# Kernel tuning notes

Hardware: AMD Instinct MI355X
Metric: run time of the kernel (lower is better)

Reference implementation:

```python
import jax, jax.numpy as jnp
import numpy as np

NB, HD, NL, NF = 5, 64, 4, 10           # num_bins, hidden_dim(d_model), num_layers, num_frames
DI, DS, DC, DTR = 128, 16, 4, 4          # d_inner=2*HD, d_state, d_conv, dt_rank=ceil(HD/16)
B, H, W = 4, 64, 64


def _conv2d(x, w, b):
    y = jax.lax.conv_general_dilated(x, w, (1, 1), 'SAME',
                                     dimension_numbers=('NCHW', 'OIHW', 'NCHW'))
    return y + b[None, :, None, None]


def _bn_relu(x, gamma, beta, eps=1e-5):
    # BatchNorm2d in training mode: biased batch stats over (N,H,W)
    mean = x.mean(axis=(0, 2, 3), keepdims=True)
    var = x.var(axis=(0, 2, 3), keepdims=True)
    y = (x - mean) * jax.lax.rsqrt(var + eps)
    return jax.nn.relu(y * gamma[None, :, None, None] + beta[None, :, None, None])


def _silu(x):
    return x * jax.nn.sigmoid(x)


def _causal_dwconv(x, w, b):
    # x: (B,L,DI), w: (DI,K) depthwise causal conv, b: (DI,)
    K = w.shape[1]
    L = x.shape[1]
    xp = jnp.pad(x, ((0, 0), (K - 1, 0), (0, 0)))
    y = sum(xp[:, k:k + L, :] * w[:, k] for k in range(K))
    return y + b


def _selective_scan(u, delta, A, Bm, Cm, D):
    # u,delta: (B,L,DI); A: (DI,DS); Bm,Cm: (B,L,DS); D: (DI,)
    dT, BT, CT, uT = (t.transpose(1, 0, 2) for t in (delta, Bm, Cm, u))
    h0 = jnp.zeros((u.shape[0], A.shape[0], A.shape[1]), u.dtype)

    def step(h, inp):
        d_t, B_t, C_t, u_t = inp                     # (B,DI),(B,DS),(B,DS),(B,DI)
        dA = jnp.exp(d_t[:, :, None] * A)            # (B,DI,DS)
        h = dA * h + (d_t * u_t)[:, :, None] * B_t[:, None, :]
        y = jnp.einsum('bds,bs->bd', h, C_t)
        return h, y

    _, ys = jax.lax.scan(step, h0, (dT, BT, CT, uT))  # ys: (L,B,DI)
    return ys.transpose(1, 0, 2) + u * D


def _mamba(x, in_proj, conv_w, conv_b, x_proj, dt_w, dt_b, A_log, Dp, out_proj):
    xz = x @ in_proj.T                               # (B,L,2*DI)
    xi, z = jnp.split(xz, 2, axis=-1)
    xi = _silu(_causal_dwconv(xi, conv_w, conv_b))
    xdbc = xi @ x_proj.T                             # (B,L,DTR+2*DS)
    dt, Bm, Cm = jnp.split(xdbc, [DTR, DTR + DS], axis=-1)
    delta = jax.nn.softplus(dt @ dt_w.T + dt_b)
    A = -jnp.exp(A_log)
    y = _selective_scan(xi, delta, A, Bm, Cm, Dp)
    return (y * _silu(z)) @ out_proj.T


def setup_inputs() -> dict:
    key = jax.random.key(0)
    ks = jax.random.split(key, 20)
    s = 0.02
    inp = {
        'x': jax.random.normal(ks[0], (B, NB, H, W), jnp.float32),
        'enc_w': jax.random.normal(ks[1], (HD, NB, 3, 3), jnp.float32) * s,
        'enc_b': jnp.zeros((HD,), jnp.float32),
        'enc_g': jnp.ones((HD,), jnp.float32),
        'enc_be': jnp.zeros((HD,), jnp.float32),
        'in_proj': jax.random.normal(ks[2], (NL, 2 * DI, HD), jnp.float32) * s,
        'conv_w': jax.random.normal(ks[3], (NL, DI, DC), jnp.float32) * s,
        'conv_b': jnp.zeros((NL, DI), jnp.float32),
        'x_proj': jax.random.normal(ks[4], (NL, DTR + 2 * DS, DI), jnp.float32) * s,
        'dt_w': jax.random.normal(ks[5], (NL, DI, DTR), jnp.float32) * s,
        'dt_b': jax.random.normal(ks[6], (NL, DI), jnp.float32) * 0.1 - 4.0,
        'A_log': jnp.broadcast_to(jnp.log(jnp.arange(1, DS + 1, dtype=jnp.float32)),
                                  (NL, DI, DS)).copy(),
        'Dp': jnp.ones((NL, DI), jnp.float32),
        'out_proj': jax.random.normal(ks[7], (NL, HD, DI), jnp.float32) * s,
        'dec1_w': jax.random.normal(ks[8], (HD, HD, 3, 3), jnp.float32) * s,
        'dec1_b': jnp.zeros((HD,), jnp.float32),
        'dec1_g': jnp.ones((HD,), jnp.float32),
        'dec1_be': jnp.zeros((HD,), jnp.float32),
        'dec2_w': jax.random.normal(ks[9], (NF, HD, 3, 3), jnp.float32) * s,
        'dec2_b': jnp.zeros((NF,), jnp.float32),
    }
    return inp


def reference(x, enc_w, enc_b, enc_g, enc_be, in_proj, conv_w, conv_b, x_proj,
              dt_w, dt_b, A_log, Dp, out_proj, dec1_w, dec1_b, dec1_g, dec1_be,
              dec2_w, dec2_b):
    Bb, _, Hh, Ww = x.shape
    h = _bn_relu(_conv2d(x, enc_w, enc_b), enc_g, enc_be)   # (B,HD,H,W)
    t = h.reshape(Bb, HD, Hh * Ww).transpose(0, 2, 1)        # (B,L,HD)
    for i in range(NL):
        t = t + _mamba(t, in_proj[i], conv_w[i], conv_b[i], x_proj[i],
                       dt_w[i], dt_b[i], A_log[i], Dp[i], out_proj[i])
    h = t.transpose(0, 2, 1).reshape(Bb, HD, Hh, Ww)
    h = _bn_relu(_conv2d(h, dec1_w, dec1_b), dec1_g, dec1_be)
    return _conv2d(h, dec2_w, dec2_b)                        # (B,NF,H,W)
```

## Files before the change

kernel.cpp:

```cpp
#include <hip/hip_runtime.h>
#include <hip/hip_bf16.h>

#define BB   4
#define NBC  5
#define HD   64
#define NLAYER 4
#define NFC  10
#define DIM  128
#define DSN  16
#define DCN  4
#define DTRK 4
#define HH   64
#define WWD  64
#define LL   4096
#define MM   (BB*LL)
#define SUB    16
#define NSUB   256
#define WIN    19

__global__ void k_prep_all(const float* __restrict__ in_proj, const float* __restrict__ out_proj,
                           const float* __restrict__ dec1_w, const float* __restrict__ dec2_w,
                           float* __restrict__ wTin, float* __restrict__ wTout,
                           float* __restrict__ wT1, float* __restrict__ wT2,
                           float* __restrict__ stats, float* __restrict__ stats2) {
    int idx = blockIdx.x * blockDim.x + threadIdx.x;
    if (idx < 65536) {
        int n = idx & 255, k = (idx >> 8) & 63, l = idx >> 14;
        wTin[idx] = in_proj[(l << 14) + (n << 6) + k];
    } else if (idx < 98304) {
        int j = idx - 65536;
        int n = j & 63, k = (j >> 6) & 127, l = j >> 13;
        wTout[j] = out_proj[(l << 13) + (n << 7) + k];
    } else if (idx < 135168) {
        int j = idx - 98304;
        int co = j & 63, tap = (j >> 6) % 9, ci = j / 576;
        wT1[j] = dec1_w[co * 576 + ci * 9 + tap];
    } else if (idx < 142848) {
        int j = idx - 135168;
        int tap = j % 12, t2 = j / 12, co = t2 % NFC, ci = t2 / NFC;
        wT2[j] = (tap < 9) ? dec2_w[co * 576 + ci * 9 + tap] : 0.f;
    } else if (idx < 143104) {
        int j = idx - 142848;
        if (j < 128) stats[j] = 0.f; else stats2[j - 128] = 0.f;
    }
}

__global__ void k_enc_conv(const float* __restrict__ x, const float* __restrict__ w,
                           const float* __restrict__ bias, float* __restrict__ out,
                           float* __restrict__ stats) {
    __shared__ float r1[256], r2[256];
    int tid = threadIdx.x;
// ... 64 lines not shown
    int rg = tid >> 5;
    int cg = tid & 31;
    float acc[8][8] = {};
    int n0 = cg << 3;
    for (int k4 = 0; k4 < 16; ++k4) {
        float4 a[8];
        #pragma unroll
        for (int r2 = 0; r2 < 8; ++r2)
            a[r2] = *(const float4*)&ts[((rg << 3) + r2) * 68 + (k4 << 2)];
        #pragma unroll
        for (int kk = 0; kk < 4; ++kk) {
            const float* wr = wT + (((k4 << 2) + kk) << 8) + n0;
            float4 w0 = *(const float4*)&wr[0];
            float4 w1 = *(const float4*)&wr[4];
            #pragma unroll
            for (int r2 = 0; r2 < 8; ++r2) {
                float av = (kk == 0) ? a[r2].x : (kk == 1) ? a[r2].y
                         : (kk == 2) ? a[r2].z : a[r2].w;
                acc[r2][0] += av * w0.x; acc[r2][1] += av * w0.y;
                acc[r2][2] += av * w0.z; acc[r2][3] += av * w0.w;
                acc[r2][4] += av * w1.x; acc[r2][5] += av * w1.y;
                acc[r2][6] += av * w1.z; acc[r2][7] += av * w1.w;
            }
        }
    }
    #pragma unroll
    for (int r2 = 0; r2 < 8; ++r2) {
        long m = m0 + (rg << 3) + r2;
        *(float4*)&xz[(m << 8) + n0]     = make_float4(acc[r2][0], acc[r2][1], acc[r2][2], acc[r2][3]);
        *(float4*)&xz[(m << 8) + n0 + 4] = make_float4(acc[r2][4], acc[r2][5], acc[r2][6], acc[r2][7]);
    }
}

__global__ __launch_bounds__(256, 3) void k_xproj_fused(
        const float* __restrict__ xz, const float* __restrict__ cw,
        const float* __restrict__ cb, const float* __restrict__ Wx,
        const float* __restrict__ dw, const float* __restrict__ dbias,
        const float* __restrict__ A_log,
        float* __restrict__ xi, float* __restrict__ delta,
        float* __restrict__ xdbc, float* __restrict__ Pb, float* __restrict__ Sb) {
    __shared__ __align__(16) float xz_s[WIN * 128];
    __shared__ __align__(16) float xi_s[SUB * 128];
    __shared__ __align__(16) float w_s[36 * 132];
    __shared__ __align__(16) float xs[SUB * 36];
    long m0 = (long)blockIdx.x << 4;
    int l0 = (int)(m0 & 4095);
    int b = (int)(m0 >> 12);
    int sc = l0 >> 4;
    int tid = threadIdx.x;

    for (int i = tid; i < WIN * 32; i += 256) {
        int j = i >> 5, c4 = (i & 31) << 2;
        float4 v = make_float4(0.f, 0.f, 0.f, 0.f);
        int l = l0 - 3 + j;
        if (l >= 0) v = *(const float4*)&xz[(m0 - 3 + j) * 256 + c4];
        *(float4*)&xz_s[j * 128 + c4] = v;
    }
    for (int i = tid; i < 1152; i += 256) {
        int n = i >> 5, c4 = (i & 31) << 2;
        *(float4*)&w_s[n * 132 + c4] = *(const float4*)&Wx[(n << 7) + c4];
    }
    int d4c = (tid & 31) << 2;
    float4 cwv0 = *(const float4*)&cw[(d4c + 0) << 2];
    float4 cwv1 = *(const float4*)&cw[(d4c + 1) << 2];
    float4 cwv2 = *(const float4*)&cw[(d4c + 2) << 2];
    float4 cwv3 = *(const float4*)&cw[(d4c + 3) << 2];
    float4 cbv  = *(const float4*)&cb[d4c];
    __syncthreads();

    #pragma unroll
    for (int ii = 0; ii < 2; ++ii) {
        int r = (tid >> 5) + (ii << 3);
        float4 x0 = *(const float4*)&xz_s[(r + 0) * 128 + d4c];
        float4 x1 = *(const float4*)&xz_s[(r + 1) * 128 + d4c];
        float4 x2 = *(const float4*)&xz_s[(r + 2) * 128 + d4c];
        float4 x3 = *(const float4*)&xz_s[(r + 3) * 128 + d4c];
        float4 a;
        a.x = cbv.x + x0.x * cwv0.x + x1.x * cwv0.y + x2.x * cwv0.z + x3.x * cwv0.w;
        a.y = cbv.y + x0.y * cwv1.x + x1.y * cwv1.y + x2.y * cwv1.z + x3.y * cwv1.w;
        a.z = cbv.z + x0.z * cwv2.x + x1.z * cwv2.y + x2.z * cwv2.z + x3.z * cwv2.w;
        a.w = cbv.w + x0.w * cwv3.x + x1.w * cwv3.y + x2.w * cwv3.z + x3.w * cwv3.w;
        a.x = a.x / (1.f + __expf(-a.x));
        a.y = a.y / (1.f + __expf(-a.y));
        a.z = a.z / (1.f + __expf(-a.z));
        a.w = a.w / (1.f + __expf(-a.w));
        *(float4*)&xi_s[r * 128 + d4c] = a;
        *(float4*)&xi[(m0 + r) * 128 + d4c] = a;
    }
    __syncthreads();

    {
        int n = tid & 63, rg6 = tid >> 6;
        if (n < 36) {
            float acc[4] = {0, 0, 0, 0};
            for (int k4 = 0; k4 < 32; ++k4) {
                float4 w4 = *(const float4*)&w_s[n * 132 + (k4 << 2)];
                #pragma unroll
                for (int r = 0; r < 4; ++r) {
                    float4 a4 = *(const float4*)&xi_s[((rg6 << 2) + r) * 128 + (k4 << 2)];
                    acc[r] += a4.x * w4.x + a4.y * w4.y + a4.z * w4.z + a4.w * w4.w;
                }
            }
            #pragma unroll
            for (int r = 0; r < 4; ++r) {
                int rr = (rg6 << 2) + r;
                xdbc[(m0 + rr) * 36 + n] = acc[r];
                xs[rr * 36 + n] = acc[r];
            }
        }
    }
    __syncthreads();

    float* delta_s = xz_s;
    for (int i = tid; i < SUB * 128; i += 256) {
        int r = i >> 7, di2 = i & 127;
        float4 d4 = *(const float4*)&dw[di2 << 2];
        float v = dbias[di2]
                + xs[r * 36 + 0] * d4.x + xs[r * 36 + 1] * d4.y
                + xs[r * 36 + 2] * d4.z + xs[r * 36 + 3] * d4.w;
        float sp = (v > 20.f) ? v : log1pf(expf(v));
        delta_s[r * 128 + di2] = sp;
        delta[(m0 + r) * 128 + di2] = sp;
    }
    __syncthreads();

    {
        int di = tid >> 1;
        int dso = (tid & 1) << 3;
        float4 al0 = *(const float4*)&A_log[(di << 4) + dso];
        float4 al1 = *(const float4*)&A_log[(di << 4) + dso + 4];
        float Av[8] = { -expf(al0.x), -expf(al0.y), -expf(al0.z), -expf(al0.w),
                        -expf(al1.x), -expf(al1.y), -expf(al1.z), -expf(al1.w) };
        float h[8] = {0,0,0,0,0,0,0,0};
        float P[8] = {1,1,1,1,1,1,1,1};
        #pragma unroll 4
        for (int i = 0; i < SUB; ++i) {
            float d = delta_s[i * 128 + di];
            float u = xi_s[i * 128 + di];
            float du = d * u;
            float4 B0 = *(const float4*)&xs[i * 36 + DTRK + dso];
            float4 B1 = *(const float4*)&xs[i * 36 + DTRK + dso + 4];
            float a0 = __expf(d * Av[0]); h[0] = a0 * h[0] + du * B0.x; P[0] *= a0;
            float a1 = __expf(d * Av[1]); h[1] = a1 * h[1] + du * B0.y; P[1] *= a1;
            float a2 = __expf(d * Av[2]); h[2] = a2 * h[2] + du * B0.z; P[2] *= a2;
            float a3 = __expf(d * Av[3]); h[3] = a3 * h[3] + du * B0.w; P[3] *= a3;
            float a4 = __expf(d * Av[4]); h[4] = a4 * h[4] + du * B1.x; P[4] *= a4;
            float a5 = __expf(d * Av[5]); h[5] = a5 * h[5] + du * B1.y; P[5] *= a5;
            float a6 = __expf(d * Av[6]); h[6] = a6 * h[6] + du * B1.z; P[6] *= a6;
            float a7 = __expf(d * Av[7]); h[7] = a7 * h[7] + du * B1.w; P[7] *= a7;
        }
        long o = (((long)(b * NSUB + sc)) << 11) + (di << 4) + dso;
        *(float4*)&Pb[o]     = make_float4(P[0], P[1], P[2], P[3]);
        *(float4*)&Pb[o + 4] = make_float4(P[4], P[5], P[6], P[7]);
        *(float4*)&Sb[o]     = make_float4(h[0], h[1], h[2], h[3]);
        *(float4*)&Sb[o + 4] = make_float4(h[4], h[5], h[6], h[7]);
    }
}

__global__ void k_scan_p2(const float* __restrict__ Pb, float* Sb) {
    int t = blockIdx.x * blockDim.x + threadIdx.x;
    int b = t >> 11;
    int s = t & 2047;
    long base = ((long)b * NSUB) << 11;
    float p[4], sv[4];
    #pragma unroll
    for (int k = 0; k < 4; ++k) {
        long idx = base + ((long)k << 11) + s;
        p[k] = Pb[idx]; sv[k] = Sb[idx];
    }
    float h = 0.f;
    for (int c = 0; c < 64; ++c) {
        float np[4] = {0, 0, 0, 0}, ns[4] = {0, 0, 0, 0};
        if (c < 63) {
            #pragma unroll
            for (int k = 0; k < 4; ++k) {
                long idx = base + ((long)(((c + 1) << 2) + k) << 11) + s;
                np[k] = Pb[idx]; ns[k] = Sb[idx];
            }
        }
        long i0 = base + ((long)(c << 2) << 11) + s;
        Sb[i0]        = h;  h = p[0] * h + sv[0];
        Sb[i0 + 2048] = h;  h = p[1] * h + sv[1];
        Sb[i0 + 4096] = h;  h = p[2] * h + sv[2];
        Sb[i0 + 6144] = h;  h = p[3] * h + sv[3];
        #pragma unroll
        for (int k = 0; k < 4; ++k) { p[k] = np[k]; sv[k] = ns[k]; }
    }
}

__global__ __launch_bounds__(256, 4) void k_scan_p3_oi(
        float* xz, const float* __restrict__ xi, const float* __restrict__ delta,
        const float* __restrict__ xdbc,
        const float* __restrict__ A_log, const float* __restrict__ Dp,
        const float* __restrict__ wTo, const float* __restrict__ wTi,
        float* __restrict__ tio, const float* __restrict__ h0g, int doB) {
    __shared__ __align__(16) float d_s[SUB * 128];
    __shared__ __align__(16) float u_s[SUB * 132];
    __shared__ __align__(16) float bc_s[SUB * 36];
    __shared__ __align__(16) float t_s[SUB * 68];
    long m0 = (long)blockIdx.x << 4;
    int tid = threadIdx.x;
    int fb = blockIdx.x;

    for (int i = tid; i < SUB * 32; i += 256) {
        int r = i >> 5, c4 = (i & 31) << 2;
        *(float4*)&d_s[r * 128 + c4] = *(const float4*)&delta[(m0 + r) * 128 + c4];
        *(float4*)&u_s[r * 132 + c4] = *(const float4*)&xi[(m0 + r) * 128 + c4];
    }
    for (int i = tid; i < SUB * 9; i += 256) {
        int r = i / 9, c4 = (i - r * 9) << 2;
        *(float4*)&bc_s[r * 36 + c4] = *(const float4*)&xdbc[(m0 + r) * 36 + c4];
    }
    int di = tid >> 1;
    int dso = (tid & 1) << 3;
    float4 al0 = *(const float4*)&A_log[(di << 4) + dso];
    float4 al1 = *(const float4*)&A_log[(di << 4) + dso + 4];
    float Av[8] = { -expf(al0.x), -expf(al0.y), -expf(al0.z), -expf(al0.w),
                    -expf(al1.x), -expf(al1.y), -expf(al1.z), -expf(al1.w) };
    float Dv = Dp[di];
    long o = (((long)fb) << 11) + (di << 4) + dso;
    float4 h04 = *(const float4*)&h0g[o];
    float4 h14 = *(const float4*)&h0g[o + 4];
    float h[8] = { h04.x, h04.y, h04.z, h04.w, h14.x, h14.y, h14.z, h14.w };
    __syncthreads();

    #pragma unroll 4
    for (int i = 0; i < SUB; ++i) {
        float d = d_s[i * 128 + di];
        float u = u_s[i * 132 + di];
        float du = d * u;
        const float* bc = &bc_s[i * 36];
        float4 B0 = *(const float4*)&bc[DTRK + dso];
        float4 B1 = *(const float4*)&bc[DTRK + dso + 4];
        float4 C0 = *(const float4*)&bc[DTRK + DSN + dso];
        float4 C1 = *(const float4*)&bc[DTRK + DSN + dso + 4];
        float a0 = __expf(d * Av[0]); h[0] = a0 * h[0] + du * B0.x;
        float a1 = __expf(d * Av[1]); h[1] = a1 * h[1] + du * B0.y;
        float a2 = __expf(d * Av[2]); h[2] = a2 * h[2] + du * B0.z;
        float a3 = __expf(d * Av[3]); h[3] = a3 * h[3] + du * B0.w;
        float a4 = __expf(d * Av[4]); h[4] = a4 * h[4] + du * B1.x;
        float a5 = __expf(d * Av[5]); h[5] = a5 * h[5] + du * B1.y;
        float a6 = __expf(d * Av[6]); h[6] = a6 * h[6] + du * B1.z;
        float a7 = __expf(d * Av[7]); h[7] = a7 * h[7] + du * B1.w;
        float yp = h[0] * C0.x + h[1] * C0.y + h[2] * C0.z + h[3] * C0.w
                 + h[4] * C1.x + h[5] * C1.y + h[6] * C1.z + h[7] * C1.w;
        yp += __shfl_xor(yp, 1);
        if (dso == 0)
            u_s[i * 132 + di] = yp + u * Dv;
    }
    __syncthreads();

    for (int i = tid; i < SUB * 32; i += 256) {
        int r = i >> 5, c4 = (i & 31) << 2;
        float4 y4 = *(float4*)&u_s[r * 132 + c4];
        float4 z4 = *(const float4*)&xz[((m0 + r) << 8) + DIM + c4];
        y4.x *= z4.x / (1.f + __expf(-z4.x));
        y4.y *= z4.y / (1.f + __expf(-z4.y));
        y4.z *= z4.z / (1.f + __expf(-z4.z));
        y4.w *= z4.w / (1.f + __expf(-z4.w));
        *(float4*)&u_s[r * 132 + c4] = y4;
    }
    __syncthreads();

    {
        int rg = tid >> 4, cg = tid & 15;
        int n0 = cg << 2;
        float acc4[4] = {};
        for (int k4 = 0; k4 < 32; ++k4) {
            float4 a0 = *(const float4*)&u_s[rg * 132 + (k4 << 2)];
            #pragma unroll
            for (int kk = 0; kk < 4; ++kk) {
                const float* wr = wTo + (((k4 << 2) + kk) << 6) + n0;
                float4 w0 = *(const float4*)&wr[0];
                float av = (kk == 0) ? a0.x : (kk == 1) ? a0.y : (kk == 2) ? a0.z : a0.w;
                acc4[0] += av * w0.x; acc4[1] += av * w0.y;
                acc4[2] += av * w0.z; acc4[3] += av * w0.w;
            }
        }
        long m = m0 + rg;
        float4 tv = *(const float4*)&tio[(m << 6) + n0];
        tv.x += acc4[0]; tv.y += acc4[1];
        tv.z += acc4[2]; tv.w += acc4[3];
        *(float4*)&tio[(m << 6) + n0] = tv;
        *(float4*)&t_s[rg * 68 + n0] = tv;
    }
    if (!doB) return;
    __syncthreads();

    {
        int rg = tid >> 5, cgn = tid & 31;
        int n0 = cgn << 3;
        float acc[2][8] = {};
        for (int k4 = 0; k4 < 16; ++k4) {
            float4 a[2];
            a[0] = *(const float4*)&t_s[(rg << 1) * 68 + (k4 << 2)];
            a[1] = *(const float4*)&t_s[((rg << 1) + 1) * 68 + (k4 << 2)];
            #pragma unroll
            for (int kk = 0; kk < 4; ++kk) {
                const float* wr = wTi + (((k4 << 2) + kk) << 8) + n0;
                float4 w0 = *(const float4*)&wr[0];
                float4 w1 = *(const float4*)&wr[4];
                #pragma unroll
                for (int r2 = 0; r2 < 2; ++r2) {
                    float av = (kk == 0) ? a[r2].x : (kk == 1) ? a[r2].y
                             : (kk == 2) ? a[r2].z : a[r2].w;
                    acc[r2][0] += av * w0.x; acc[r2][1] += av * w0.y;
                    acc[r2][2] += av * w0.z; acc[r2][3] += av * w0.w;
                    acc[r2][4] += av * w1.x; acc[r2][5] += av * w1.y;
                    acc[r2][6] += av * w1.z; acc[r2][7] += av * w1.w;
                }
            }
        }
        #pragma unroll
        for (int r2 = 0; r2 < 2; ++r2) {
            long m = m0 + (rg << 1) + r2;
            *(float4*)&xz[(m << 8) + n0]     = make_float4(acc[r2][0], acc[r2][1], acc[r2][2], acc[r2][3]);
            *(float4*)&xz[(m << 8) + n0 + 4] = make_float4(acc[r2][4], acc[r2][5], acc[r2][6], acc[r2][7]);
        }
    }
}

__global__ __launch_bounds__(256, 1) void k_dec1_new(const float* __restrict__ tin,
                                                     const float* __restrict__ wT,
                                                     const float* __restrict__ bias,
                                                     float* __restrict__ out,
                                                     float* __restrict__ stats2) {
    __shared__ __align__(16) float x_s[64 * 132];
    __shared__ __align__(16) float w_s[4 * 4608];
    int tile = blockIdx.x;
    int b = blockIdx.y;
    int ty0 = (tile >> 3) << 3;
    int tx0 = (tile & 7) << 3;
    int tid = threadIdx.x;
    int wv = tid >> 6;
    int lane = tid & 63;
    int r = lane >> 3;
    int cg = lane & 7;

    for (int i = tid; i < 6400; i += 256) {
        int pl = i >> 6;
        int c = i & 63;
        int py = pl / 10, px = pl - py * 10;
        int ih = ty0 + py - 1, iw = tx0 + px - 1;
        float v = 0.f;
        if (ih >= 0 && ih < HH && iw >= 0 && iw < WWD)
            v = tin[(((long)((b << 12) + (ih << 6) + iw)) << 6) + c];
        x_s[c * 132 + py * 12 + px] = v;
    }
    float* myw = &w_s[wv * 4608];
    const float* gw = wT + (wv * 16) * 576;
    float4 pref[18];
// ... 166 lines not shown
    const float* x       = (const float*)d_in[0];
    const float* enc_w   = (const float*)d_in[1];
    const float* enc_b   = (const float*)d_in[2];
    const float* enc_g   = (const float*)d_in[3];
    const float* enc_be  = (const float*)d_in[4];
    const float* in_proj = (const float*)d_in[5];
    const float* conv_w  = (const float*)d_in[6];
    const float* conv_b  = (const float*)d_in[7];
    const float* x_proj  = (const float*)d_in[8];
    const float* dt_w    = (const float*)d_in[9];
    const float* dt_b    = (const float*)d_in[10];
    const float* A_log   = (const float*)d_in[11];
    const float* Dp      = (const float*)d_in[12];
    const float* out_prj = (const float*)d_in[13];
    const float* dec1_w  = (const float*)d_in[14];
    const float* dec1_b  = (const float*)d_in[15];
    const float* dec1_g  = (const float*)d_in[16];
    const float* dec1_be = (const float*)d_in[17];
    const float* dec2_w  = (const float*)d_in[18];
    const float* dec2_b  = (const float*)d_in[19];
    float* out = (float*)d_out;

    float* ws = (float*)d_ws;
    size_t off = 0;
    float* conv_buf  = ws + off; off += 1048576;
    float* stats     = ws + off; off += 128;
    float* stats2    = ws + off; off += 128;
    float* wT1       = ws + off; off += 36864;
    float* wT2       = ws + off; off += 7680;
    float* wTin      = ws + off; off += 65536;
    float* wTout     = ws + off; off += 32768;
    float* t_buf     = ws + off; off += 1048576;
    float* xz_buf    = ws + off; off += 4194304;
    float* xi_buf    = ws + off; off += 2097152;
    float* delta_buf = ws + off; off += 2097152;
    float* xdbc_buf  = ws + off; off += 589824;
    float* Pb        = ws + off; off += 2097152;
    float* Sb        = ws + off; off += 2097152;
    (void)ws_size; (void)in_sizes; (void)n_in; (void)out_size;

    k_prep_all<<<560, 256, 0, stream>>>(in_proj, out_prj, dec1_w, dec2_w,
                                        wTin, wTout, wT1, wT2, stats, stats2);

    k_enc_conv<<<4096, 256, 0, stream>>>(x, enc_w, enc_b, conv_buf, stats);

    k_gemm_in_bn<<<256, 256, 0, stream>>>(conv_buf, stats, enc_g, enc_be, wTin,
                                          t_buf, xz_buf);

    for (int i = 0; i < NLAYER; ++i) {
        int doB = (i < NLAYER - 1) ? 1 : 0;
        k_xproj_fused<<<1024, 256, 0, stream>>>(
            xz_buf, conv_w + i * DIM * DCN, conv_b + i * DIM, x_proj + i * 36 * DIM,
            dt_w + i * DIM * DTRK, dt_b + i * DIM, A_log + i * DIM * DSN,
            xi_buf, delta_buf, xdbc_buf, Pb, Sb);
        k_scan_p2<<<32, 256, 0, stream>>>(Pb, Sb);
        k_scan_p3_oi<<<1024, 256, 0, stream>>>(
            xz_buf, xi_buf, delta_buf, xdbc_buf,
            A_log + i * DIM * DSN, Dp + i * DIM,
            wTout + i * 8192, wTin + ((i + 1) & 3) * 16384,
            t_buf, Sb, doB);
    }

    dim3 dg1(64, BB);
    k_dec1_new<<<dg1, 256, 0, stream>>>(t_buf, wT1, dec1_b, conv_buf, stats2);
    k_dec2_fused<<<dg1, 256, 0, stream>>>(conv_buf, stats2, dec1_g, dec1_be, wT2, dec2_b, out);
}
```

Measured before the change: 547.4 us.

## Halve scan chunk size to double block count and fuse gating into scan loop

Shrinks the per-block sequence chunk from 16 to 8 rows, so the x-projection and scan-output kernels launch twice as many blocks. The x_proj weight staging in shared memory is dropped in favour of direct global reads, and occupancy hints are raised. The SiLU(z) gating is folded into the scan loop using a preloaded z tile, which removes a separate pass and a barrier. In exchange, the serial carry-propagation kernel walks twice as many chunks, the prefix buffers double in size, and weight reuse per block falls.

```diff
diff --git a/kernel.cpp b/kernel.cpp
--- a/kernel.cpp
+++ b/kernel.cpp
@@ -14,9 +14,9 @@
 #define WWD  64
 #define LL   4096
 #define MM   (BB*LL)
-#define SUB    16
-#define NSUB   256
-#define WIN    19
+#define SUB    8
+#define NSUB   512
+#define WIN    11
 
 __global__ void k_prep_all(const float* __restrict__ in_proj, const float* __restrict__ out_proj,
                            const float* __restrict__ dec1_w, const float* __restrict__ dec2_w,
@@ -147,7 +147,7 @@
     }
 }
 
-__global__ __launch_bounds__(256, 3) void k_xproj_fused(
+__global__ __launch_bounds__(256, 4) void k_xproj_fused(
         const float* __restrict__ xz, const float* __restrict__ cw,
         const float* __restrict__ cb, const float* __restrict__ Wx,
         const float* __restrict__ dw, const float* __restrict__ dbias,
@@ -156,12 +156,9 @@
         float* __restrict__ xdbc, float* __restrict__ Pb, float* __restrict__ Sb) {
     __shared__ __align__(16) float xz_s[WIN * 128];
     __shared__ __align__(16) float xi_s[SUB * 128];
-    __shared__ __align__(16) float w_s[36 * 132];
     __shared__ __align__(16) float xs[SUB * 36];
-    long m0 = (long)blockIdx.x << 4;
+    long m0 = (long)blockIdx.x << 3;
     int l0 = (int)(m0 & 4095);
-    int b = (int)(m0 >> 12);
-    int sc = l0 >> 4;
     int tid = threadIdx.x;
 
     for (int i = tid; i < WIN * 32; i += 256) {
@@ -171,10 +168,6 @@
         if (l >= 0) v = *(const float4*)&xz[(m0 - 3 + j) * 256 + c4];
         *(float4*)&xz_s[j * 128 + c4] = v;
     }
-    for (int i = tid; i < 1152; i += 256) {
-        int n = i >> 5, c4 = (i & 31) << 2;
-        *(float4*)&w_s[n * 132 + c4] = *(const float4*)&Wx[(n << 7) + c4];
-    }
     int d4c = (tid & 31) << 2;
     float4 cwv0 = *(const float4*)&cw[(d4c + 0) << 2];
     float4 cwv1 = *(const float4*)&cw[(d4c + 1) << 2];
@@ -183,9 +176,8 @@
     float4 cbv  = *(const float4*)&cb[d4c];
     __syncthreads();
 
-    #pragma unroll
-    for (int ii = 0; ii < 2; ++ii) {
-        int r = (tid >> 5) + (ii << 3);
+    {
+        int r = tid >> 5;
         float4 x0 = *(const float4*)&xz_s[(r + 0) * 128 + d4c];
         float4 x1 = *(const float4*)&xz_s[(r + 1) * 128 + d4c];
         float4 x2 = *(const float4*)&xz_s[(r + 2) * 128 + d4c];
@@ -207,18 +199,18 @@
     {
         int n = tid & 63, rg6 = tid >> 6;
         if (n < 36) {
-            float acc[4] = {0, 0, 0, 0};
+            float acc[2] = {0, 0};
             for (int k4 = 0; k4 < 32; ++k4) {
-                float4 w4 = *(const float4*)&w_s[n * 132 + (k4 << 2)];
+                float4 w4 = *(const float4*)&Wx[(n << 7) + (k4 << 2)];
                 #pragma unroll
-                for (int r = 0; r < 4; ++r) {
-                    float4 a4 = *(const float4*)&xi_s[((rg6 << 2) + r) * 128 + (k4 << 2)];
+                for (int r = 0; r < 2; ++r) {
+                    float4 a4 = *(const float4*)&xi_s[((rg6 << 1) + r) * 128 + (k4 << 2)];
                     acc[r] += a4.x * w4.x + a4.y * w4.y + a4.z * w4.z + a4.w * w4.w;
                 }
             }
             #pragma unroll
-            for (int r = 0; r < 4; ++r) {
-                int rr = (rg6 << 2) + r;
+            for (int r = 0; r < 2; ++r) {
+                int rr = (rg6 << 1) + r;
                 xdbc[(m0 + rr) * 36 + n] = acc[r];
                 xs[rr * 36 + n] = acc[r];
             }
@@ -248,7 +240,7 @@
                         -expf(al1.x), -expf(al1.y), -expf(al1.z), -expf(al1.w) };
         float h[8] = {0,0,0,0,0,0,0,0};
         float P[8] = {1,1,1,1,1,1,1,1};
-        #pragma unroll 4
+        #pragma unroll
         for (int i = 0; i < SUB; ++i) {
             float d = delta_s[i * 128 + di];
             float u = xi_s[i * 128 + di];
@@ -264,7 +256,7 @@
             float a6 = __expf(d * Av[6]); h[6] = a6 * h[6] + du * B1.z; P[6] *= a6;
             float a7 = __expf(d * Av[7]); h[7] = a7 * h[7] + du * B1.w; P[7] *= a7;
         }
-        long o = (((long)(b * NSUB + sc)) << 11) + (di << 4) + dso;
+        long o = ((long)blockIdx.x << 11) + (di << 4) + dso;
         *(float4*)&Pb[o]     = make_float4(P[0], P[1], P[2], P[3]);
         *(float4*)&Pb[o + 4] = make_float4(P[4], P[5], P[6], P[7]);
         *(float4*)&Sb[o]     = make_float4(h[0], h[1], h[2], h[3]);
@@ -284,9 +276,9 @@
         p[k] = Pb[idx]; sv[k] = Sb[idx];
     }
     float h = 0.f;
-    for (int c = 0; c < 64; ++c) {
+    for (int c = 0; c < 128; ++c) {
         float np[4] = {0, 0, 0, 0}, ns[4] = {0, 0, 0, 0};
-        if (c < 63) {
+        if (c < 127) {
             #pragma unroll
             for (int k = 0; k < 4; ++k) {
                 long idx = base + ((long)(((c + 1) << 2) + k) << 11) + s;
@@ -311,19 +303,20 @@
         float* __restrict__ tio, const float* __restrict__ h0g, int doB) {
     __shared__ __align__(16) float d_s[SUB * 128];
     __shared__ __align__(16) float u_s[SUB * 132];
+    __shared__ __align__(16) float z_s[SUB * 132];
     __shared__ __align__(16) float bc_s[SUB * 36];
     __shared__ __align__(16) float t_s[SUB * 68];
-    long m0 = (long)blockIdx.x << 4;
+    long m0 = (long)blockIdx.x << 3;
     int tid = threadIdx.x;
-    int fb = blockIdx.x;
-
-    for (int i = tid; i < SUB * 32; i += 256) {
-        int r = i >> 5, c4 = (i & 31) << 2;
+
+    {
+        int r = tid >> 5, c4 = (tid & 31) << 2;
         *(float4*)&d_s[r * 128 + c4] = *(const float4*)&delta[(m0 + r) * 128 + c4];
         *(float4*)&u_s[r * 132 + c4] = *(const float4*)&xi[(m0 + r) * 128 + c4];
-    }
-    for (int i = tid; i < SUB * 9; i += 256) {
-        int r = i / 9, c4 = (i - r * 9) << 2;
+        *(float4*)&z_s[r * 132 + c4] = *(const float4*)&xz[((m0 + r) << 8) + DIM + c4];
+    }
+    if (tid < SUB * 9) {
+        int r = tid / 9, c4 = (tid - r * 9) << 2;
         *(float4*)&bc_s[r * 36 + c4] = *(const float4*)&xdbc[(m0 + r) * 36 + c4];
     }
     int di = tid >> 1;
@@ -333,13 +326,13 @@
     float Av[8] = { -expf(al0.x), -expf(al0.y), -expf(al0.z), -expf(al0.w),
                     -expf(al1.x), -expf(al1.y), -expf(al1.z), -expf(al1.w) };
     float Dv = Dp[di];
-    long o = (((long)fb) << 11) + (di << 4) + dso;
+    long o = ((long)blockIdx.x << 11) + (di << 4) + dso;
     float4 h04 = *(const float4*)&h0g[o];
     float4 h14 = *(const float4*)&h0g[o + 4];
     float h[8] = { h04.x, h04.y, h04.z, h04.w, h14.x, h14.y, h14.z, h14.w };
     __syncthreads();
 
-    #pragma unroll 4
+    #pragma unroll
     for (int i = 0; i < SUB; ++i) {
         float d = d_s[i * 128 + di];
         float u = u_s[i * 132 + di];
@@ -360,44 +353,32 @@
         float yp = h[0] * C0.x + h[1] * C0.y + h[2] * C0.z + h[3] * C0.w
                  + h[4] * C1.x + h[5] * C1.y + h[6] * C1.z + h[7] * C1.w;
         yp += __shfl_xor(yp, 1);
-        if (dso == 0)
-            u_s[i * 132 + di] = yp + u * Dv;
-    }
-    __syncthreads();
-
-    for (int i = tid; i < SUB * 32; i += 256) {
-        int r = i >> 5, c4 = (i & 31) << 2;
-        float4 y4 = *(float4*)&u_s[r * 132 + c4];
-        float4 z4 = *(const float4*)&xz[((m0 + r) << 8) + DIM + c4];
-        y4.x *= z4.x / (1.f + __expf(-z4.x));
-        y4.y *= z4.y / (1.f + __expf(-z4.y));
-        y4.z *= z4.z / (1.f + __expf(-z4.z));
-        y4.w *= z4.w / (1.f + __expf(-z4.w));
-        *(float4*)&u_s[r * 132 + c4] = y4;
+        if (dso == 0) {
+            float z = z_s[i * 132 + di];
+            u_s[i * 132 + di] = (yp + u * Dv) * (z / (1.f + __expf(-z)));
+        }
     }
     __syncthreads();
 
     {
-        int rg = tid >> 4, cg = tid & 15;
-        int n0 = cg << 2;
-        float acc4[4] = {};
+        int rg = tid >> 5, cg = tid & 31;
+        int n0 = cg << 1;
+        float acc2[2] = {0.f, 0.f};
         for (int k4 = 0; k4 < 32; ++k4) {
             float4 a0 = *(const float4*)&u_s[rg * 132 + (k4 << 2)];
             #pragma unroll
             for (int kk = 0; kk < 4; ++kk) {
                 const float* wr = wTo + (((k4 << 2) + kk) << 6) + n0;
-                float4 w0 = *(const float4*)&wr[0];
+                float2 w0 = *(const float2*)&wr[0];
                 float av = (kk == 0) ? a0.x : (kk == 1) ? a0.y : (kk == 2) ? a0.z : a0.w;
-                acc4[0] += av * w0.x; acc4[1] += av * w0.y;
-                acc4[2] += av * w0.z; acc4[3] += av * w0.w;
+                acc2[0] += av * w0.x; acc2[1] += av * w0.y;
             }
         }
         long m = m0 + rg;
-        float4 tv = *(const float4*)&tio[(m << 6) + n0];
-        tv.x += acc4[0]; tv.y += acc4[1];
-        tv.z += acc4[2]; tv.w += acc4[3];
-        *(float4*)&tio[(m << 6) + n0] = tv;
-        *(float4*)&t_s[rg * 68 + n0] = tv;
+        float2 tv = *(const float2*)&tio[(m << 6) + n0];
+        tv.x += acc2[0]; tv.y += acc2[1];
+        *(float2*)&tio[(m << 6) + n0] = tv;
+        *(float2*)&t_s[rg * 68 + n0] = tv;
     }
     if (!doB) return;
     __syncthreads();
@@ -405,33 +386,24 @@
     {
         int rg = tid >> 5, cgn = tid & 31;
         int n0 = cgn << 3;
-        float acc[2][8] = {};
+        float acc[8] = {};
         for (int k4 = 0; k4 < 16; ++k4) {
-            float4 a[2];
-            a[0] = *(const float4*)&t_s[(rg << 1) * 68 + (k4 << 2)];
-            a[1] = *(const float4*)&t_s[((rg << 1) + 1) * 68 + (k4 << 2)];
+            float4 a0 = *(const float4*)&t_s[rg * 68 + (k4 << 2)];
             #pragma unroll
             for (int kk = 0; kk < 4; ++kk) {
                 const float* wr = wTi + (((k4 << 2) + kk) << 8) + n0;
                 float4 w0 = *(const float4*)&wr[0];
                 float4 w1 = *(const float4*)&wr[4];
-                #pragma unroll
-                for (int r2 = 0; r2 < 2; ++r2) {
-                    float av = (kk == 0) ? a[r2].x : (kk == 1) ? a[r2].y
-                             : (kk == 2) ? a[r2].z : a[r2].w;
-                    acc[r2][0] += av * w0.x; acc[r2][1] += av * w0.y;
-                    acc[r2][2] += av * w0.z; acc[r2][3] += av * w0.w;
-                    acc[r2][4] += av * w1.x; acc[r2][5] += av * w1.y;
-                    acc[r2][6] += av * w1.z; acc[r2][7] += av * w1.w;
-                }
-            }
-        }
-        #pragma unroll
-        for (int r2 = 0; r2 < 2; ++r2) {
-            long m = m0 + (rg << 1) + r2;
-            *(float4*)&xz[(m << 8) + n0]     = make_float4(acc[r2][0], acc[r2][1], acc[r2][2], acc[r2][3]);
-            *(float4*)&xz[(m << 8) + n0 + 4] = make_float4(acc[r2][4], acc[r2][5], acc[r2][6], acc[r2][7]);
-        }
+                float av = (kk == 0) ? a0.x : (kk == 1) ? a0.y : (kk == 2) ? a0.z : a0.w;
+                acc[0] += av * w0.x; acc[1] += av * w0.y;
+                acc[2] += av * w0.z; acc[3] += av * w0.w;
+                acc[4] += av * w1.x; acc[5] += av * w1.y;
+                acc[6] += av * w1.z; acc[7] += av * w1.w;
+            }
+        }
+        long m = m0 + rg;
+        *(float4*)&xz[(m << 8) + n0]     = make_float4(acc[0], acc[1], acc[2], acc[3]);
+        *(float4*)&xz[(m << 8) + n0 + 4] = make_float4(acc[4], acc[5], acc[6], acc[7]);
     }
 }
 
@@ -667,8 +639,8 @@
     float* xi_buf    = ws + off; off += 2097152;
     float* delta_buf = ws + off; off += 2097152;
     float* xdbc_buf  = ws + off; off += 589824;
-    float* Pb        = ws + off; off += 2097152;
-    float* Sb        = ws + off; off += 2097152;
+    float* Pb        = ws + off; off += 4194304;
+    float* Sb        = ws + off; off += 4194304;
     (void)ws_size; (void)in_sizes; (void)n_in; (void)out_size;
 
     k_prep_all<<<560, 256, 0, stream>>>(in_proj, out_prj, dec1_w, dec2_w,
@@ -681,12 +653,12 @@
 
     for (int i = 0; i < NLAYER; ++i) {
         int doB = (i < NLAYER - 1) ? 1 : 0;
-        k_xproj_fused<<<1024, 256, 0, stream>>>(
+        k_xproj_fused<<<2048, 256, 0, stream>>>(
             xz_buf, conv_w + i * DIM * DCN, conv_b + i * DIM, x_proj + i * 36 * DIM,
             dt_w + i * DIM * DTRK, dt_b + i * DIM, A_log + i * DIM * DSN,
             xi_buf, delta_buf, xdbc_buf, Pb, Sb);
         k_scan_p2<<<32, 256, 0, stream>>>(Pb, Sb);
-        k_scan_p3_oi<<<1024, 256, 0, stream>>>(
+        k_scan_p3_oi<<<2048, 256, 0, stream>>>(
             xz_buf, xi_buf, delta_buf, xdbc_buf,
             A_log + i * DIM * DSN, Dp + i * DIM,
             wTout + i * 8192, wTin + ((i + 1) & 3) * 16384,
```

Measured after the change: 744.1 us. 1.36x slower.

## Double scan chunk length and store delta/xi transposed for register-held scan inputs

Applied to the files above, without the earlier changes.

The chunk length of the chunked selective scan goes from 16 to 32 rows, which halves the number of chunks, the grid sizes and the Pb/Sb carry buffers. The xproj kernel now uses 512-thread blocks and writes delta and xi in a column-major (channel-major) layout. This lets the final scan kernel load each channel's 32 values straight into registers and trade them between lane pairs with shuffles instead of staging them in shared memory. It also fuses the SiLU(z) gate into the scan loop and widens the per-thread row tiles of the out_proj and in_proj GEMMs. The risks are strided global stores for the transposed buffers, a longer serial scan per block, and less parallelism across blocks.

```diff
diff --git a/kernel.cpp b/kernel.cpp
--- a/kernel.cpp
+++ b/kernel.cpp
@@ -14,9 +14,11 @@
 #define WWD  64
 #define LL   4096
 #define MM   (BB*LL)
-#define SUB    16
-#define NSUB   256
-#define WIN    19
+#define CLEN   32
+#define NCHUNK 128
+
+#define A4GET(a, i) (((i) & 3) == 0 ? (a)[(i) >> 2].x : ((i) & 3) == 1 ? (a)[(i) >> 2].y : \
+                     ((i) & 3) == 2 ? (a)[(i) >> 2].z : (a)[(i) >> 2].w)
 
 __global__ void k_prep_all(const float* __restrict__ in_proj, const float* __restrict__ out_proj,
                            const float* __restrict__ dec1_w, const float* __restrict__ dec2_w,
@@ -147,60 +149,54 @@
     }
 }
 
-__global__ __launch_bounds__(256, 3) void k_xproj_fused(
+__global__ __launch_bounds__(512, 4) void k_xproj_fused(
         const float* __restrict__ xz, const float* __restrict__ cw,
         const float* __restrict__ cb, const float* __restrict__ Wx,
         const float* __restrict__ dw, const float* __restrict__ dbias,
         const float* __restrict__ A_log,
-        float* __restrict__ xi, float* __restrict__ delta,
+        float* __restrict__ xiT, float* __restrict__ deltaT,
         float* __restrict__ xdbc, float* __restrict__ Pb, float* __restrict__ Sb) {
-    __shared__ __align__(16) float xz_s[WIN * 128];
-    __shared__ __align__(16) float xi_s[SUB * 128];
+    __shared__ __align__(16) float xz_s[35 * 132];
+    __shared__ __align__(16) float xi_s[32 * 132];
     __shared__ __align__(16) float w_s[36 * 132];
-    __shared__ __align__(16) float xs[SUB * 36];
-    long m0 = (long)blockIdx.x << 4;
+    __shared__ __align__(16) float xs[32 * 40];
+    __shared__ float cwT[4 * 128];
+    __shared__ float cb_s[128];
+    long m0 = (long)blockIdx.x << 5;
     int l0 = (int)(m0 & 4095);
-    int b = (int)(m0 >> 12);
-    int sc = l0 >> 4;
     int tid = threadIdx.x;
 
-    for (int i = tid; i < WIN * 32; i += 256) {
+    for (int i = tid; i < 35 * 32; i += 512) {
         int j = i >> 5, c4 = (i & 31) << 2;
         float4 v = make_float4(0.f, 0.f, 0.f, 0.f);
-        int l = l0 - 3 + j;
-        if (l >= 0) v = *(const float4*)&xz[(m0 - 3 + j) * 256 + c4];
-        *(float4*)&xz_s[j * 128 + c4] = v;
-    }
-    for (int i = tid; i < 1152; i += 256) {
+        if (l0 - 3 + j >= 0) v = *(const float4*)&xz[(m0 - 3 + j) * 256 + c4];
+        *(float4*)&xz_s[j * 132 + c4] = v;
+    }
+    if (tid < 128) cb_s[tid] = cb[tid];
+    { int kk = tid >> 7, dii = tid & 127; if (tid < 512) cwT[(kk << 7) + dii] = cw[(dii << 2) + kk]; }
+    for (int i = tid; i < 1152; i += 512) {
         int n = i >> 5, c4 = (i & 31) << 2;
         *(float4*)&w_s[n * 132 + c4] = *(const float4*)&Wx[(n << 7) + c4];
     }
-    int d4c = (tid & 31) << 2;
-    float4 cwv0 = *(const float4*)&cw[(d4c + 0) << 2];
-    float4 cwv1 = *(const float4*)&cw[(d4c + 1) << 2];
-    float4 cwv2 = *(const float4*)&cw[(d4c + 2) << 2];
-    float4 cwv3 = *(const float4*)&cw[(d4c + 3) << 2];
-    float4 cbv  = *(const float4*)&cb[d4c];
     __syncthreads();
 
     #pragma unroll
     for (int ii = 0; ii < 2; ++ii) {
-        int r = (tid >> 5) + (ii << 3);
-        float4 x0 = *(const float4*)&xz_s[(r + 0) * 128 + d4c];
-        float4 x1 = *(const float4*)&xz_s[(r + 1) * 128 + d4c];
-        float4 x2 = *(const float4*)&xz_s[(r + 2) * 128 + d4c];
-        float4 x3 = *(const float4*)&xz_s[(r + 3) * 128 + d4c];
-        float4 a;
-        a.x = cbv.x + x0.x * cwv0.x + x1.x * cwv0.y + x2.x * cwv0.z + x3.x * cwv0.w;
-        a.y = cbv.y + x0.y * cwv1.x + x1.y * cwv1.y + x2.y * cwv1.z + x3.y * cwv1.w;
-        a.z = cbv.z + x0.z * cwv2.x + x1.z * cwv2.y + x2.z * cwv2.z + x3.z * cwv2.w;
-        a.w = cbv.w + x0.w * cwv3.x + x1.w * cwv3.y + x2.w * cwv3.z + x3.w * cwv3.w;
+        int i = tid + (ii << 9);
+        int r = i >> 5, d4 = (i & 31) << 2;
+        float4 a = *(const float4*)&cb_s[d4];
+        #pragma unroll
+        for (int kk = 0; kk < 4; ++kk) {
+            float4 xv = *(const float4*)&xz_s[(r + kk) * 132 + d4];
+            float4 wv = *(const float4*)&cwT[(kk << 7) + d4];
+            a.x += xv.x * wv.x; a.y += xv.y * wv.y;
+            a.z += xv.z * wv.z; a.w += xv.w * wv.w;
+        }
         a.x = a.x / (1.f + __expf(-a.x));
         a.y = a.y / (1.f + __expf(-a.y));
         a.z = a.z / (1.f + __expf(-a.z));
         a.w = a.w / (1.f + __expf(-a.w));
-        *(float4*)&xi_s[r * 128 + d4c] = a;
-        *(float4*)&xi[(m0 + r) * 128 + d4c] = a;
+        *(float4*)&xi_s[r * 132 + d4] = a;
     }
     __syncthreads();
 
@@ -212,7 +208,7 @@
                 float4 w4 = *(const float4*)&w_s[n * 132 + (k4 << 2)];
                 #pragma unroll
                 for (int r = 0; r < 4; ++r) {
-                    float4 a4 = *(const float4*)&xi_s[((rg6 << 2) + r) * 128 + (k4 << 2)];
+                    float4 a4 = *(const float4*)&xi_s[((rg6 << 2) + r) * 132 + (k4 << 2)];
                     acc[r] += a4.x * w4.x + a4.y * w4.y + a4.z * w4.z + a4.w * w4.w;
                 }
             }
@@ -220,55 +216,60 @@
             for (int r = 0; r < 4; ++r) {
                 int rr = (rg6 << 2) + r;
                 xdbc[(m0 + rr) * 36 + n] = acc[r];
-                xs[rr * 36 + n] = acc[r];
+                xs[rr * 40 + n] = acc[r];
             }
         }
     }
     __syncthreads();
 
     float* delta_s = xz_s;
-    for (int i = tid; i < SUB * 128; i += 256) {
+    for (int i = tid; i < 4096; i += 512) {
         int r = i >> 7, di2 = i & 127;
         float4 d4 = *(const float4*)&dw[di2 << 2];
         float v = dbias[di2]
-                + xs[r * 36 + 0] * d4.x + xs[r * 36 + 1] * d4.y
-                + xs[r * 36 + 2] * d4.z + xs[r * 36 + 3] * d4.w;
+                + xs[r * 40 + 0] * d4.x + xs[r * 40 + 1] * d4.y
+                + xs[r * 40 + 2] * d4.z + xs[r * 40 + 3] * d4.w;
         float sp = (v > 20.f) ? v : log1pf(expf(v));
-        delta_s[r * 128 + di2] = sp;
-        delta[(m0 + r) * 128 + di2] = sp;
+        delta_s[r * 132 + di2] = sp;
     }
     __syncthreads();
 
     {
-        int di = tid >> 1;
-        int dso = (tid & 1) << 3;
-        float4 al0 = *(const float4*)&A_log[(di << 4) + dso];
-        float4 al1 = *(const float4*)&A_log[(di << 4) + dso + 4];
-        float Av[8] = { -expf(al0.x), -expf(al0.y), -expf(al0.z), -expf(al0.w),
-                        -expf(al1.x), -expf(al1.y), -expf(al1.z), -expf(al1.w) };
-        float h[8] = {0,0,0,0,0,0,0,0};
-        float P[8] = {1,1,1,1,1,1,1,1};
+        int dii = tid & 127, q = tid >> 7;
+        float td[8], tu[8];
+        #pragma unroll
+        for (int j = 0; j < 8; ++j) {
+            td[j] = delta_s[((q << 3) + j) * 132 + dii];
+            tu[j] = xi_s[((q << 3) + j) * 132 + dii];
+        }
+        long tb = (long)dii * MM + m0 + (q << 3);
+        *(float4*)&deltaT[tb]     = make_float4(td[0], td[1], td[2], td[3]);
+        *(float4*)&deltaT[tb + 4] = make_float4(td[4], td[5], td[6], td[7]);
+        *(float4*)&xiT[tb]        = make_float4(tu[0], tu[1], tu[2], tu[3]);
+        *(float4*)&xiT[tb + 4]    = make_float4(tu[4], tu[5], tu[6], tu[7]);
+    }
+
+    {
+        int di = tid >> 2;
+        int dso = (tid & 3) << 2;
+        float4 al = *(const float4*)&A_log[(di << 4) + dso];
+        float Av[4] = { -expf(al.x), -expf(al.y), -expf(al.z), -expf(al.w) };
+        float h[4] = {0, 0, 0, 0};
+        float P[4] = {1, 1, 1, 1};
         #pragma unroll 4
-        for (int i = 0; i < SUB; ++i) {
-            float d = delta_s[i * 128 + di];
-            float u = xi_s[i * 128 + di];
+        for (int i = 0; i < CLEN; ++i) {
+            float d = delta_s[i * 132 + di];
+            float u = xi_s[i * 132 + di];
             float du = d * u;
-            float4 B0 = *(const float4*)&xs[i * 36 + DTRK + dso];
-            float4 B1 = *(const float4*)&xs[i * 36 + DTRK + dso + 4];
+            float4 B0 = *(const float4*)&xs[i * 40 + DTRK + dso];
             float a0 = __expf(d * Av[0]); h[0] = a0 * h[0] + du * B0.x; P[0] *= a0;
             float a1 = __expf(d * Av[1]); h[1] = a1 * h[1] + du * B0.y; P[1] *= a1;
             float a2 = __expf(d * Av[2]); h[2] = a2 * h[2] + du * B0.z; P[2] *= a2;
             float a3 = __expf(d * Av[3]); h[3] = a3 * h[3] + du * B0.w; P[3] *= a3;
-            float a4 = __expf(d * Av[4]); h[4] = a4 * h[4] + du * B1.x; P[4] *= a4;
-            float a5 = __expf(d * Av[5]); h[5] = a5 * h[5] + du * B1.y; P[5] *= a5;
-            float a6 = __expf(d * Av[6]); h[6] = a6 * h[6] + du * B1.z; P[6] *= a6;
-            float a7 = __expf(d * Av[7]); h[7] = a7 * h[7] + du * B1.w; P[7] *= a7;
-        }
-        long o = (((long)(b * NSUB + sc)) << 11) + (di << 4) + dso;
-        *(float4*)&Pb[o]     = make_float4(P[0], P[1], P[2], P[3]);
-        *(float4*)&Pb[o + 4] = make_float4(P[4], P[5], P[6], P[7]);
-        *(float4*)&Sb[o]     = make_float4(h[0], h[1], h[2], h[3]);
-        *(float4*)&Sb[o + 4] = make_float4(h[4], h[5], h[6], h[7]);
+        }
+        long o = ((long)blockIdx.x << 11) + (di << 4) + dso;
+        *(float4*)&Pb[o] = make_float4(P[0], P[1], P[2], P[3]);
+        *(float4*)&Sb[o] = make_float4(h[0], h[1], h[2], h[3]);
     }
 }
 
@@ -276,7 +277,7 @@
     int t = blockIdx.x * blockDim.x + threadIdx.x;
     int b = t >> 11;
     int s = t & 2047;
-    long base = ((long)b * NSUB) << 11;
+    long base = (long)b << 18;
     float p[4], sv[4];
     #pragma unroll
     for (int k = 0; k < 4; ++k) {
@@ -284,9 +285,9 @@
         p[k] = Pb[idx]; sv[k] = Sb[idx];
     }
     float h = 0.f;
-    for (int c = 0; c < 64; ++c) {
+    for (int c = 0; c < 32; ++c) {
         float np[4] = {0, 0, 0, 0}, ns[4] = {0, 0, 0, 0};
-        if (c < 63) {
+        if (c < 31) {
             #pragma unroll
             for (int k = 0; k < 4; ++k) {
                 long idx = base + ((long)(((c + 1) << 2) + k) << 11) + s;
@@ -304,45 +305,52 @@
 }
 
 __global__ __launch_bounds__(256, 4) void k_scan_p3_oi(
-        float* xz, const float* __restrict__ xi, const float* __restrict__ delta,
+        float* xz, const float* __restrict__ xiT, const float* __restrict__ deltaT,
         const float* __restrict__ xdbc,
         const float* __restrict__ A_log, const float* __restrict__ Dp,
         const float* __restrict__ wTo, const float* __restrict__ wTi,
         float* __restrict__ tio, const float* __restrict__ h0g, int doB) {
-    __shared__ __align__(16) float d_s[SUB * 128];
-    __shared__ __align__(16) float u_s[SUB * 132];
-    __shared__ __align__(16) float bc_s[SUB * 36];
-    __shared__ __align__(16) float t_s[SUB * 68];
-    long m0 = (long)blockIdx.x << 4;
+    __shared__ __align__(16) float u_s[CLEN * 132];
+    __shared__ __align__(16) float bc_s[CLEN * 36];
+    __shared__ __align__(16) float t_s[CLEN * 68];
+    long m0 = (long)blockIdx.x << 5;
     int tid = threadIdx.x;
-    int fb = blockIdx.x;
-
-    for (int i = tid; i < SUB * 32; i += 256) {
+    int di = tid >> 1;
+    int odd = tid & 1;
+    int dso = odd << 3;
+
+    const float* colp = (odd ? xiT : deltaT) + (long)di * MM + m0;
+    float4 a4[8];
+    #pragma unroll
+    for (int j = 0; j < 8; ++j) a4[j] = *(const float4*)&colp[j << 2];
+
+    #pragma unroll
+    for (int ii = 0; ii < 4; ++ii) {
+        int i = tid + (ii << 8);
         int r = i >> 5, c4 = (i & 31) << 2;
-        *(float4*)&d_s[r * 128 + c4] = *(const float4*)&delta[(m0 + r) * 128 + c4];
-        *(float4*)&u_s[r * 132 + c4] = *(const float4*)&xi[(m0 + r) * 128 + c4];
-    }
-    for (int i = tid; i < SUB * 9; i += 256) {
+        *(float4*)&u_s[r * 132 + c4] = *(const float4*)&xz[((m0 + r) << 8) + DIM + c4];
+    }
+    for (int i = tid; i < CLEN * 9; i += 256) {
         int r = i / 9, c4 = (i - r * 9) << 2;
         *(float4*)&bc_s[r * 36 + c4] = *(const float4*)&xdbc[(m0 + r) * 36 + c4];
     }
-    int di = tid >> 1;
-    int dso = (tid & 1) << 3;
     float4 al0 = *(const float4*)&A_log[(di << 4) + dso];
     float4 al1 = *(const float4*)&A_log[(di << 4) + dso + 4];
     float Av[8] = { -expf(al0.x), -expf(al0.y), -expf(al0.z), -expf(al0.w),
                     -expf(al1.x), -expf(al1.y), -expf(al1.z), -expf(al1.w) };
     float Dv = Dp[di];
-    long o = (((long)fb) << 11) + (di << 4) + dso;
+    long o = ((long)blockIdx.x << 11) + (di << 4) + dso;
     float4 h04 = *(const float4*)&h0g[o];
     float4 h14 = *(const float4*)&h0g[o + 4];
     float h[8] = { h04.x, h04.y, h04.z, h04.w, h14.x, h14.y, h14.z, h14.w };
     __syncthreads();
 
-    #pragma unroll 4
-    for (int i = 0; i < SUB; ++i) {
-        float d = d_s[i * 128 + di];
-        float u = u_s[i * 132 + di];
+    #pragma unroll
+    for (int i = 0; i < CLEN; ++i) {
+        float own = A4GET(a4, i);
+        float oth = __shfl_xor(own, 1);
+        float d = odd ? oth : own;
+        float u = odd ? own : oth;
         float du = d * u;
         const float* bc = &bc_s[i * 36];
         float4 B0 = *(const float4*)&bc[DTRK + dso];
@@ -353,51 +361,48 @@
         float a1 = __expf(d * Av[1]); h[1] = a1 * h[1] + du * B0.y;
         float a2 = __expf(d * Av[2]); h[2] = a2 * h[2] + du * B0.z;
         float a3 = __expf(d * Av[3]); h[3] = a3 * h[3] + du * B0.w;
-        float a4 = __expf(d * Av[4]); h[4] = a4 * h[4] + du * B1.x;
+        float a4s = __expf(d * Av[4]); h[4] = a4s * h[4] + du * B1.x;
         float a5 = __expf(d * Av[5]); h[5] = a5 * h[5] + du * B1.y;
         float a6 = __expf(d * Av[6]); h[6] = a6 * h[6] + du * B1.z;
         float a7 = __expf(d * Av[7]); h[7] = a7 * h[7] + du * B1.w;
         float yp = h[0] * C0.x + h[1] * C0.y + h[2] * C0.z + h[3] * C0.w
                  + h[4] * C1.x + h[5] * C1.y + h[6] * C1.z + h[7] * C1.w;
         yp += __shfl_xor(yp, 1);
-        if (dso == 0)
-            u_s[i * 132 + di] = yp + u * Dv;
-    }
-    __syncthreads();
-
-    for (int i = tid; i < SUB * 32; i += 256) {
-        int r = i >> 5, c4 = (i & 31) << 2;
-        float4 y4 = *(float4*)&u_s[r * 132 + c4];
-        float4 z4 = *(const float4*)&xz[((m0 + r) << 8) + DIM + c4];
-        y4.x *= z4.x / (1.f + __expf(-z4.x));
-        y4.y *= z4.y / (1.f + __expf(-z4.y));
-        y4.z *= z4.z / (1.f + __expf(-z4.z));
-        y4.w *= z4.w / (1.f + __expf(-z4.w));
-        *(float4*)&u_s[r * 132 + c4] = y4;
+        if (!odd) {
+            float z = u_s[i * 132 + di];
+            u_s[i * 132 + di] = (yp + u * Dv) * (z / (1.f + __expf(-z)));
+        }
     }
     __syncthreads();
 
     {
         int rg = tid >> 4, cg = tid & 15;
         int n0 = cg << 2;
-        float acc4[4] = {};
+        float acc[2][4] = {};
         for (int k4 = 0; k4 < 32; ++k4) {
-            float4 a0 = *(const float4*)&u_s[rg * 132 + (k4 << 2)];
+            float4 a0 = *(const float4*)&u_s[(rg << 1) * 132 + (k4 << 2)];
+            float4 a1 = *(const float4*)&u_s[((rg << 1) + 1) * 132 + (k4 << 2)];
             #pragma unroll
             for (int kk = 0; kk < 4; ++kk) {
                 const float* wr = wTo + (((k4 << 2) + kk) << 6) + n0;
                 float4 w0 = *(const float4*)&wr[0];
-                float av = (kk == 0) ? a0.x : (kk == 1) ? a0.y : (kk == 2) ? a0.z : a0.w;
-                acc4[0] += av * w0.x; acc4[1] += av * w0.y;
-                acc4[2] += av * w0.z; acc4[3] += av * w0.w;
-            }
-        }
-        long m = m0 + rg;
-        float4 tv = *(const float4*)&tio[(m << 6) + n0];
-        tv.x += acc4[0]; tv.y += acc4[1];
-        tv.z += acc4[2]; tv.w += acc4[3];
-        *(float4*)&tio[(m << 6) + n0] = tv;
-        *(float4*)&t_s[rg * 68 + n0] = tv;
+                float av0 = (kk == 0) ? a0.x : (kk == 1) ? a0.y : (kk == 2) ? a0.z : a0.w;
+                float av1 = (kk == 0) ? a1.x : (kk == 1) ? a1.y : (kk == 2) ? a1.z : a1.w;
+                acc[0][0] += av0 * w0.x; acc[0][1] += av0 * w0.y;
+                acc[0][2] += av0 * w0.z; acc[0][3] += av0 * w0.w;
+                acc[1][0] += av1 * w0.x; acc[1][1] += av1 * w0.y;
+                acc[1][2] += av1 * w0.z; acc[1][3] += av1 * w0.w;
+            }
+        }
+        #pragma unroll
+        for (int r2 = 0; r2 < 2; ++r2) {
+            long m = m0 + (rg << 1) + r2;
+            float4 tv = *(const float4*)&tio[(m << 6) + n0];
+            tv.x += acc[r2][0]; tv.y += acc[r2][1];
+            tv.z += acc[r2][2]; tv.w += acc[r2][3];
+            *(float4*)&tio[(m << 6) + n0] = tv;
+            *(float4*)&t_s[((rg << 1) + r2) * 68 + n0] = tv;
+        }
     }
     if (!doB) return;
     __syncthreads();
@@ -405,18 +410,19 @@
     {
         int rg = tid >> 5, cgn = tid & 31;
         int n0 = cgn << 3;
-        float acc[2][8] = {};
+        float acc[4][8] = {};
         for (int k4 = 0; k4 < 16; ++k4) {
-            float4 a[2];
-            a[0] = *(const float4*)&t_s[(rg << 1) * 68 + (k4 << 2)];
-            a[1] = *(const float4*)&t_s[((rg << 1) + 1) * 68 + (k4 << 2)];
+            float4 a[4];
+            #pragma unroll
+            for (int r2 = 0; r2 < 4; ++r2)
+                a[r2] = *(const float4*)&t_s[((rg << 2) + r2) * 68 + (k4 << 2)];
             #pragma unroll
             for (int kk = 0; kk < 4; ++kk) {
                 const float* wr = wTi + (((k4 << 2) + kk) << 8) + n0;
                 float4 w0 = *(const float4*)&wr[0];
                 float4 w1 = *(const float4*)&wr[4];
                 #pragma unroll
-                for (int r2 = 0; r2 < 2; ++r2) {
+                for (int r2 = 0; r2 < 4; ++r2) {
                     float av = (kk == 0) ? a[r2].x : (kk == 1) ? a[r2].y
                              : (kk == 2) ? a[r2].z : a[r2].w;
                     acc[r2][0] += av * w0.x; acc[r2][1] += av * w0.y;
@@ -427,8 +433,8 @@
             }
         }
         #pragma unroll
-        for (int r2 = 0; r2 < 2; ++r2) {
-            long m = m0 + (rg << 1) + r2;
+        for (int r2 = 0; r2 < 4; ++r2) {
+            long m = m0 + (rg << 2) + r2;
             *(float4*)&xz[(m << 8) + n0]     = make_float4(acc[r2][0], acc[r2][1], acc[r2][2], acc[r2][3]);
             *(float4*)&xz[(m << 8) + n0 + 4] = make_float4(acc[r2][4], acc[r2][5], acc[r2][6], acc[r2][7]);
         }
@@ -664,11 +670,11 @@
     float* wTout     = ws + off; off += 32768;
     float* t_buf     = ws + off; off += 1048576;
     float* xz_buf    = ws + off; off += 4194304;
-    float* xi_buf    = ws + off; off += 2097152;
-    float* delta_buf = ws + off; off += 2097152;
+    float* xiT_buf   = ws + off; off += 2097152;
+    float* deltaT_buf= ws + off; off += 2097152;
     float* xdbc_buf  = ws + off; off += 589824;
-    float* Pb        = ws + off; off += 2097152;
-    float* Sb        = ws + off; off += 2097152;
+    float* Pb        = ws + off; off += 1048576;
+    float* Sb        = ws + off; off += 1048576;
     (void)ws_size; (void)in_sizes; (void)n_in; (void)out_size;
 
     k_prep_all<<<560, 256, 0, stream>>>(in_proj, out_prj, dec1_w, dec2_w,
@@ -681,13 +687,13 @@
 
     for (int i = 0; i < NLAYER; ++i) {
         int doB = (i < NLAYER - 1) ? 1 : 0;
-        k_xproj_fused<<<1024, 256, 0, stream>>>(
+        k_xproj_fused<<<512, 512, 0, stream>>>(
             xz_buf, conv_w + i * DIM * DCN, conv_b + i * DIM, x_proj + i * 36 * DIM,
             dt_w + i * DIM * DTRK, dt_b + i * DIM, A_log + i * DIM * DSN,
-            xi_buf, delta_buf, xdbc_buf, Pb, Sb);
+            xiT_buf, deltaT_buf, xdbc_buf, Pb, Sb);
         k_scan_p2<<<32, 256, 0, stream>>>(Pb, Sb);
-        k_scan_p3_oi<<<1024, 256, 0, stream>>>(
-            xz_buf, xi_buf, delta_buf, xdbc_buf,
+        k_scan_p3_oi<<<512, 256, 0, stream>>>(
+            xz_buf, xiT_buf, deltaT_buf, xdbc_buf,
             A_log + i * DIM * DSN, Dp + i * DIM,
             wTout + i * 8192, wTin + ((i + 1) & 3) * 16384,
             t_buf, Sb, doB);
```

New measurement: 502.4 us. 8.2% less time.
